# Kernel tuning notes

Measured on AMD Instinct MI355X. Metric: run time of the kernel, lower is better.

The kernel has to match this reference:

```python
import jax, jax.numpy as jnp
import numpy as np

B, C, H, W, HEADS, S = 8, 512, 32, 32, 8, 77
CH = C // HEADS  # per-head channels = 64
GROUPS = 32      # GroupNorm32


def setup_inputs() -> dict:
    key = jax.random.key(0)
    ks = jax.random.split(key, 6)
    s = 0.02
    return {
        "x": jax.random.normal(ks[0], (B, C, H, W), jnp.float32),
        "encoder_out": jax.random.normal(ks[1], (B, C, S), jnp.float32),
        "capt_attn_mask": jax.random.bernoulli(ks[2], 0.9, (B, S)),
        "norm_scale": jnp.ones((C,), jnp.float32),
        "norm_bias": jnp.zeros((C,), jnp.float32),
        "qkv_w": jax.random.normal(ks[3], (3 * C, C), jnp.float32) * s,
        "qkv_b": jnp.zeros((3 * C,), jnp.float32),
        "ekv_w": jax.random.normal(ks[4], (2 * C, C), jnp.float32) * s,
        "ekv_b": jnp.zeros((2 * C,), jnp.float32),
        "proj_w": jax.random.normal(ks[5], (C, C), jnp.float32) * s,
        "proj_b": jnp.zeros((C,), jnp.float32),
    }


def reference(x, encoder_out, capt_attn_mask, norm_scale, norm_bias,
              qkv_w, qkv_b, ekv_w, ekv_b, proj_w, proj_b):
    b, c, h, w = x.shape
    T = h * w
    xf = x.reshape(b, c, T)

    # GroupNorm(32) in fp32 (GroupNorm32), affine
    xg = xf.reshape(b, GROUPS, c // GROUPS, T).astype(jnp.float32)
    mu = xg.mean(axis=(2, 3), keepdims=True)
    var = xg.var(axis=(2, 3), keepdims=True)
    nrm = ((xg - mu) * jax.lax.rsqrt(var + 1e-5)).reshape(b, c, T)
    nrm = nrm * norm_scale[None, :, None] + norm_bias[None, :, None]

    # 1x1 conv1d qkv projection: [b, 3c, T]
    qkv = jnp.einsum('oc,bct->bot', qkv_w, nrm) + qkv_b[None, :, None]
    qkv = qkv.reshape(b * HEADS, 3 * CH, T)
    q, k, v = jnp.split(qkv, 3, axis=1)  # each [b*heads, CH, T]

    # encoder kv: [b, 2c, S] -> [b*heads, 2*CH, S]
    ekv = jnp.einsum('oc,bcs->bos', ekv_w, encoder_out) + ekv_b[None, :, None]
    ekv = ekv.reshape(b * HEADS, 2 * CH, S)
    ek, ev = jnp.split(ekv, 2, axis=1)
    k = jnp.concatenate([ek, k], axis=-1)  # [b*heads, CH, S+T]
    v = jnp.concatenate([ev, v], axis=-1)

    scale = 1.0 / np.sqrt(np.sqrt(CH))
    wgt = jnp.einsum('bct,bcs->bts', q * scale, k * scale).astype(jnp.float32)

    # additive mask; torch.tile over dim0 is head-major (row i -> batch i % b),
    # faithfully reproduced; self-attn part (last T cols) is all-visible.
    addm_capt = jnp.where(jnp.tile(capt_attn_mask, (HEADS, 1)), 0.0, -10000.0)
    addm = jnp.concatenate(
        [addm_capt, jnp.zeros((b * HEADS, T), jnp.float32)], axis=1)[:, None, :]
    wgt = jax.nn.softmax(wgt + addm, axis=-1).astype(v.dtype)

    out = jnp.einsum('bts,bcs->bct', wgt, v)  # [b*heads, CH, T]
    out = out.reshape(b, c, T)
    out = jnp.einsum('oc,bct->bot', proj_w, out) + proj_b[None, :, None]
    return (xf + out).reshape(b, c, h, w)
```

## Files before the change

kernel.cpp:

```cpp
#include <hip/hip_runtime.h>
#include <math.h>

#define BB 8
#define TT 1024
#define SS 77

typedef short v8s __attribute__((ext_vector_type(8)));
typedef float v4f __attribute__((ext_vector_type(4)));
typedef unsigned short u16x4 __attribute__((ext_vector_type(4)));
typedef unsigned short u16x8 __attribute__((ext_vector_type(8)));
typedef unsigned short u16;

#define SCALEF 0.424660891f
#define MASKNEG (-14426.95f)

__device__ __forceinline__ u16 f2bf(float f) {
  unsigned u = __float_as_uint(f);
  u = (u + 0x7fffu + ((u >> 16) & 1u)) >> 16;
  return (u16)u;
}
__device__ __forceinline__ u16 hi16(float f) {
  return (u16)(__float_as_uint(f) >> 16);
}
__device__ __forceinline__ float bf2f(u16 u) {
  return __uint_as_float(((unsigned)u) << 16);
}
__device__ __forceinline__ void gl_lds16(const void* g, void* l) {
  __builtin_amdgcn_global_load_lds(
      (const __attribute__((address_space(1))) void*)g,
      (__attribute__((address_space(3))) void*)l, 16, 0, 0);
}

__global__ __launch_bounds__(256) void prep_gn_kernel(
    const float* __restrict__ x, const float* __restrict__ scale,
    const float* __restrict__ bias, u16* __restrict__ nrmT,
    const float* __restrict__ qkv_w, const float* __restrict__ ekv_w,
    const float* __restrict__ proj_w, const float* __restrict__ enc,
    const float* __restrict__ qkv_b, const float* __restrict__ ekv_b,
    u16* __restrict__ wQK, u16* __restrict__ wV, u16* __restrict__ wEK,
    u16* __restrict__ wEV, u16* __restrict__ projwb, u16* __restrict__ encT,
    float* __restrict__ bQK, float* __restrict__ bV,
    float* __restrict__ bEK, float* __restrict__ bEV) {
  __shared__ u16 Xs[16 * 1024];
  __shared__ float red[8];
  int blk = blockIdx.x, tid = threadIdx.x;

  if (blk < 256) {
    int bg = blk;
    int b = bg >> 5, g = bg & 31;
    const float4* x4 = (const float4*)(x + (size_t)bg * 16384);
    float s = 0.f, sq = 0.f;
#pragma unroll
    for (int i = 0; i < 16; ++i) {
      int idx = tid + 256 * i;
      float4 v = x4[idx];
      s += v.x + v.y + v.z + v.w;
      sq += v.x * v.x + v.y * v.y + v.z * v.z + v.w * v.w;
      int c = idx >> 8, t4 = (idx & 255) * 4;
      u16x4 o; o.x = f2bf(v.x); o.y = f2bf(v.y); o.z = f2bf(v.z); o.w = f2bf(v.w);
      *(u16x4*)(Xs + c * 1024 + t4) = o;
    }
#pragma unroll
    for (int off = 32; off > 0; off >>= 1) {
      s += __shfl_down(s, off, 64);
      sq += __shfl_down(sq, off, 64);
    }
    int wave = tid >> 6;
    if ((tid & 63) == 0) { red[wave] = s; red[wave + 4] = sq; }
    __syncthreads();
    float ts = red[0] + red[1] + red[2] + red[3];
    float tq = red[4] + red[5] + red[6] + red[7];
    float mu = ts * (1.0f / 16384.0f);
    float var = tq * (1.0f / 16384.0f) - mu * mu;
    float rs = rsqrtf(var + 1e-5f);
    float scv[16], biv[16];
#pragma unroll
    for (int c = 0; c < 16; ++c) {
      float ss = scale[g * 16 + c] * rs;
      scv[c] = ss;
      biv[c] = bias[g * 16 + c] - mu * ss;
    }
#pragma unroll
    for (int j = 0; j < 4; ++j) {
      int t = tid + 256 * j;
      u16x8 o0, o1;
#pragma unroll
      for (int c = 0; c < 8; ++c)  o0[c] = f2bf(bf2f(Xs[c * 1024 + t]) * scv[c] + biv[c]);
#pragma unroll
      for (int c = 8; c < 16; ++c) o1[c - 8] = f2bf(bf2f(Xs[c * 1024 + t]) * scv[c] + biv[c]);
      u16* dst = nrmT + ((size_t)b * 1024 + t) * 512 + g * 16;
      *(u16x8*)dst = o0;
      *(u16x8*)(dst + 8) = o1;
    }
    return;
  }

  int p = blk - 256;
  if (p < 512) {
    int idx = p * 256 + tid;
    int n = idx >> 7, c4 = (idx & 127) * 4;
    int which = n >> 9, h = (n >> 6) & 7, ch = n & 63;
    int src = h * 192 + which * 64 + ch;
    float4 v = *(const float4*)(qkv_w + (size_t)src * 512 + c4);
    u16x4 o; o.x = f2bf(v.x * SCALEF); o.y = f2bf(v.y * SCALEF);
    o.z = f2bf(v.z * SCALEF); o.w = f2bf(v.w * SCALEF);
    *(u16x4*)(wQK + (size_t)n * 512 + c4) = o;
  } else if (p < 768) {
    int idx = (p - 512) * 256 + tid;
    int n = idx >> 7, c4 = (idx & 127) * 4;
    int h = n >> 6, ch = n & 63;
    int src = h * 192 + 128 + ch;
    float4 v = *(const float4*)(qkv_w + (size_t)src * 512 + c4);
    u16x4 o; o.x = f2bf(v.x); o.y = f2bf(v.y); o.z = f2bf(v.z); o.w = f2bf(v.w);
    *(u16x4*)(wV + (size_t)n * 512 + c4) = o;
  } else if (p < 1024) {
    int idx = (p - 768) * 256 + tid;
    int n = idx >> 7, c4 = (idx & 127) * 4;
    int h = n >> 6, ch = n & 63;
    int src = h * 128 + ch;
    float4 v = *(const float4*)(ekv_w + (size_t)src * 512 + c4);
    u16x4 o; o.x = f2bf(v.x * SCALEF); o.y = f2bf(v.y * SCALEF);
    o.z = f2bf(v.z * SCALEF); o.w = f2bf(v.w * SCALEF);
    *(u16x4*)(wEK + (size_t)n * 512 + c4) = o;
  } else if (p < 1280) {
    int idx = (p - 1024) * 256 + tid;
    int n = idx >> 7, c4 = (idx & 127) * 4;
    int h = n >> 6, ch = n & 63;
    int src = h * 128 + 64 + ch;
    float4 v = *(const float4*)(ekv_w + (size_t)src * 512 + c4);
    u16x4 o; o.x = f2bf(v.x); o.y = f2bf(v.y); o.z = f2bf(v.z); o.w = f2bf(v.w);
    *(u16x4*)(wEV + (size_t)n * 512 + c4) = o;
  } else if (p < 1536) {
    int idx = (p - 1280) * 256 + tid;
    float4 v = ((const float4*)proj_w)[idx];
    u16x4 o; o.x = f2bf(v.x); o.y = f2bf(v.y); o.z = f2bf(v.z); o.w = f2bf(v.w);
    *(u16x4*)(projwb + (size_t)idx * 4) = o;
  } else if (p < 2048) {
    int idx = (p - 1536) * 256 + tid;
    int b = idx >> 14, rem = idx & 16383;
    int s = rem >> 7, c = (rem & 127) * 4;
    u16x4 o; o.x = 0; o.y = 0; o.z = 0; o.w = 0;
    if (s < SS) {
      const float* pp = enc + ((size_t)b * 512 + c) * SS + s;
      o.x = f2bf(pp[0]); o.y = f2bf(pp[SS]); o.z = f2bf(pp[2 * SS]); o.w = f2bf(pp[3 * SS]);
    }
    *(u16x4*)(encT + ((size_t)b * 128 + s) * 512 + c) = o;
  } else {
    for (int i = tid; i < 2560; i += 256) {
      if (i < 1024) {
        int which = i >> 9, h = (i >> 6) & 7, ch = i & 63;
        bQK[i] = qkv_b[h * 192 + which * 64 + ch] * SCALEF;
      } else if (i < 1536) {
        int j = i - 1024; int h = j >> 6, ch = j & 63;
        bV[j] = qkv_b[h * 192 + 128 + ch];
      } else if (i < 2048) {
        int j = i - 1536; int h = j >> 6, ch = j & 63;
        bEK[j] = ekv_b[h * 128 + ch] * SCALEF;
      } else {
        int j = i - 2048; int h = j >> 6, ch = j & 63;
        bEV[j] = ekv_b[h * 128 + 64 + ch];
      }
    }
  }
}

__global__ __launch_bounds__(256) void proj_all(
    const u16* __restrict__ nrmT, const u16* __restrict__ encT,
    const u16* __restrict__ wQK, const u16* __restrict__ wEK,
    const u16* __restrict__ wV, const u16* __restrict__ wEV,
    const float* __restrict__ bQK, const float* __restrict__ bEK,
    const float* __restrict__ bV, const float* __restrict__ bEV,
    u16* __restrict__ Qh, u16* __restrict__ Kfull, u16* __restrict__ Vfull) {
  __shared__ __align__(16) u16 SH[16384];
  u16* As = SH;
  u16* Bs = SH + 8192;

  int job = blockIdx.x, bz = blockIdx.y;
  int tid = threadIdx.x;
  int lane = tid & 63, w = tid >> 6;
  int lan15 = lane & 15, quad = lane >> 4;
  int wm = w >> 1, wn = w & 1;

  int mode, m0, n0;
  const u16 *Ap, *Bp;
  const float* bias;
  u16 *dA = nullptr, *dB = nullptr;
  int TrA = 0, offA = 0, TrB = 0, offB = 0;
  int coff = 0;

  if (job < 64) {
    mode = 3; m0 = (job >> 3) * 128; n0 = (job & 7) * 128;
    Ap = nrmT + (size_t)bz * 1024 * 512; Bp = wQK; bias = bQK;
    dA = Qh; TrA = 1024; offA = 0; dB = Kfull; TrB = 1152; offB = 128;
  } else if (job < 68) {
    mode = 3; m0 = 0; n0 = (job - 64) * 128;
    Ap = encT + (size_t)bz * 128 * 512; Bp = wEK; bias = bEK;
    dA = Kfull; TrA = 1152; offA = 0; dB = Kfull; TrB = 1152; offB = 0;
  } else if (job < 100) {
    int jj = job - 68; mode = 0; m0 = (jj >> 3) * 128; n0 = (jj & 7) * 128;
    Ap = wV; Bp = nrmT + (size_t)bz * 1024 * 512; bias = bV;
    coff = 128;
  } else {
    int jj = job - 100; mode = 0; m0 = jj * 128; n0 = 0;
    Ap = wEV; Bp = encT + (size_t)bz * 128 * 512; bias = bEV;
    coff = 0;
  }

  int srow = lane >> 3;
  int schunk = (lane & 7) ^ srow;
  const char* Ag = (const char*)(Ap + (size_t)(m0 + w * 32 + srow) * 512) + schunk * 16;
  const char* Bg = (const char*)(Bp + (size_t)(n0 + w * 32 + srow) * 512) + schunk * 16;
  char* Al = (char*)As + w * 4096;
  char* Bl = (char*)Bs + w * 4096;

  v4f acc[4][4] = {};

  for (int step = 0; step < 8; ++step) {
    __syncthreads();
    int kb = step * 128;
#pragma unroll
    for (int i = 0; i < 4; ++i) gl_lds16(Ag + kb + i * 8192, Al + i * 1024);
#pragma unroll
    for (int i = 0; i < 4; ++i) gl_lds16(Bg + kb + i * 8192, Bl + i * 1024);
    __syncthreads();

#pragma unroll
    for (int ksub = 0; ksub < 2; ++ksub) {
      int ch = ((ksub * 4 + quad) ^ (lan15 & 7)) * 16;
      v8s a[4], bf[4];
#pragma unroll
      for (int i = 0; i < 4; ++i)
        a[i] = *(const v8s*)((const char*)As + (wm * 64 + i * 16 + lan15) * 128 + ch);
#pragma unroll
      for (int j = 0; j < 4; ++j)
        bf[j] = *(const v8s*)((const char*)Bs + (wn * 64 + j * 16 + lan15) * 128 + ch);
#pragma unroll
      for (int i = 0; i < 4; ++i)
#pragma unroll
        for (int j = 0; j < 4; ++j)
          acc[i][j] = __builtin_amdgcn_mfma_f32_16x16x32_bf16(a[i], bf[j], acc[i][j], 0, 0, 0);
    }
  }

  if (mode == 3) {
    u16* Tr = SH;
    for (int ph = 0; ph < 2; ++ph) {
      __syncthreads();
      if (wn == ph) {
#pragma unroll
        for (int j = 0; j < 4; ++j) {
          int n = n0 + wn * 64 + j * 16 + lan15;
          float bv_ = bias[n];
#pragma unroll
          for (int i = 0; i < 4; ++i)
#pragma unroll
            for (int r = 0; r < 4; ++r)
              Tr[(wm * 64 + i * 16 + quad * 4 + r) * 72 + j * 16 + lan15] =
                  f2bf(acc[i][j][r] + bv_);
        }
      }
      __syncthreads();
      int nb = n0 + ph * 64;
      u16* dst = (nb < 512) ? dA : dB;
      int Trows = (nb < 512) ? TrA : TrB;
      int roff  = (nb < 512) ? offA : offB;
      int hh = (nb & 511) >> 6;
      int row = tid >> 1, seg = (tid & 1) * 32;
      u16* dp = dst + ((size_t)(bz * 8 + hh) * Trows + roff + m0 + row) * 64 + seg;
#pragma unroll
      for (int g = 0; g < 4; ++g)
        *(u16x8*)(dp + g * 8) = *(const u16x8*)(Tr + row * 72 + seg + g * 8);
    }
  } else {
    u16* Tr = SH;
    u16* Cb = Vfull + (size_t)bz * 512 * 1152;
    for (int ph = 0; ph < 2; ++ph) {
      __syncthreads();
      if (wn == ph) {
#pragma unroll
        for (int i = 0; i < 4; ++i) {
          int ob = wm * 64 + i * 16 + quad * 4;
#pragma unroll
          for (int r = 0; r < 4; ++r) {
            float bi = bias[m0 + ob + r];
#pragma unroll
            for (int j = 0; j < 4; ++j)
              Tr[(ob + r) * 72 + j * 16 + lan15] = f2bf(acc[i][j][r] + bi);
          }
        }
      }
      __syncthreads();
      int row = tid >> 1, seg = (tid & 1) * 32;
      u16* dp = Cb + (size_t)(m0 + row) * 1152 + coff + n0 + ph * 64 + seg;
#pragma unroll
      for (int g = 0; g < 4; ++g)
        *(u16x8*)(dp + g * 8) = *(const u16x8*)(Tr + row * 72 + seg + g * 8);
    }
  }
}

__global__ __launch_bounds__(256) void proj_out(
    const u16* __restrict__ A, const u16* __restrict__ B,
    const float* __restrict__ bias, const float* __restrict__ res,
    float* __restrict__ Cf) {
  __shared__ __align__(16) u16 SH[16384];
  u16* As = SH;
  u16* Bs = SH + 8192;

  int tid = threadIdx.x;
  int lane = tid & 63, w = tid >> 6;
  int lan15 = lane & 15, quad = lane >> 4;
  int wm = w >> 1, wn = w & 1;
  int m0 = blockIdx.y * 128, n0 = blockIdx.x * 128;
  int bz = blockIdx.z;
  const u16* Bb = B + (size_t)bz * 1024 * 512;

  int srow = lane >> 3;
  int schunk = (lane & 7) ^ srow;
  const char* Ag = (const char*)(A + (size_t)(m0 + w * 32 + srow) * 512) + schunk * 16;
  const char* Bg = (const char*)(Bb + (size_t)(n0 + w * 32 + srow) * 512) + schunk * 16;
  char* Al = (char*)As + w * 4096;
  char* Bl = (char*)Bs + w * 4096;

  v4f acc[4][4] = {};

  for (int step = 0; step < 8; ++step) {
    __syncthreads();
    int kb = step * 128;
#pragma unroll
    for (int i = 0; i < 4; ++i) gl_lds16(Ag + kb + i * 8192, Al + i * 1024);
#pragma unroll
    for (int i = 0; i < 4; ++i) gl_lds16(Bg + kb + i * 8192, Bl + i * 1024);
    __syncthreads();

#pragma unroll
    for (int ksub = 0; ksub < 2; ++ksub) {
      int ch = ((ksub * 4 + quad) ^ (lan15 & 7)) * 16;
      v8s a[4], bf[4];
#pragma unroll
      for (int i = 0; i < 4; ++i)
        a[i] = *(const v8s*)((const char*)As + (wm * 64 + i * 16 + lan15) * 128 + ch);
#pragma unroll
      for (int j = 0; j < 4; ++j)
        bf[j] = *(const v8s*)((const char*)Bs + (wn * 64 + j * 16 + lan15) * 128 + ch);
#pragma unroll
      for (int i = 0; i < 4; ++i)
#pragma unroll
        for (int j = 0; j < 4; ++j)
          acc[i][j] = __builtin_amdgcn_mfma_f32_16x16x32_bf16(a[i], bf[j], acc[i][j], 0, 0, 0);
    }
  }

  const float* rb = res + (size_t)bz * 512 * 1024;
  float* Cb = Cf + (size_t)bz * 512 * 1024;
#pragma unroll
  for (int i = 0; i < 4; ++i) {
    int ob = m0 + wm * 64 + i * 16 + quad * 4;
#pragma unroll
    for (int r = 0; r < 4; ++r) {
      int o = ob + r;
      float bi = bias[o];
#pragma unroll
      for (int j = 0; j < 4; ++j) {
        int n = n0 + wn * 64 + j * 16 + lan15;
        Cb[(size_t)o * 1024 + n] = acc[i][j][r] + bi + rb[(size_t)o * 1024 + n];
      }
    }
  }
}

#define AOFF_K 0
#define AOFF_V 24576
#define AOFF_P 49152
#define AOFF_AM 67584
#define ASMEM  68096

__global__ __launch_bounds__(256) void attn_kernel(
    const u16* __restrict__ Qh, const u16* __restrict__ Kf,
    const u16* __restrict__ Vf, const int* __restrict__ mask,
    u16* __restrict__ attnT) {
  __shared__ __align__(16) unsigned char smem[ASMEM];
  float* AM = (float*)(smem + AOFF_AM);

  int bh = blockIdx.x, b = bh >> 3, h = bh & 7;
  int t0 = blockIdx.y * 128;
  int tid = threadIdx.x;
  int lane = tid & 63, w = tid >> 6;
  int lan15 = lane & 15, quad = lane >> 4;
  int r8 = lane >> 3, c8 = lane & 7;
  int swE = (c8 ^ r8) * 8;

  const u16* Qb = Qh + (size_t)bh * 1024 * 64;
  const u16* Kb = Kf + (size_t)bh * 1152 * 64;
  const u16* Vb = Vf + (size_t)bh * 64 * 1152;
  char* Pw = (char*)smem + AOFF_P + w * 4608;
  u16* Pu = (u16*)Pw;

  if (tid < 128)
    AM[tid] = (tid < SS) ? ((mask[h * SS + tid] != 0) ? 0.f : MASKNEG) : -1e30f;

#pragma unroll
  for (int i = 0; i < 4; ++i)
    gl_lds16(Qb + (size_t)(t0 + w * 32 + i * 8 + r8) * 64 + swE, Pw + i * 1024);
#pragma unroll
  for (int cc = 0; cc < 2; ++cc) {
#pragma unroll
    for (int i = 0; i < 2; ++i) {
      int row = w * 16 + i * 8;
      gl_lds16(Kb + (size_t)(cc * 64 + row + r8) * 64 + swE,
               (char*)smem + AOFF_K + cc * 8192 + row * 128);
      gl_lds16(Vb + (size_t)(row + r8) * 1152 + cc * 64 + swE,
               (char*)smem + AOFF_V + cc * 8192 + row * 128);
    }
  }

  asm volatile("s_waitcnt vmcnt(8)" ::: "memory");
  __builtin_amdgcn_sched_barrier(0);

  v8s aq[2][2];
#pragma unroll
  for (int mt = 0; mt < 2; ++mt)
#pragma unroll
    for (int ks = 0; ks < 2; ++ks)
      aq[mt][ks] = *(const v8s*)(Pw + (mt * 16 + lan15) * 128 +
                                 (((ks * 4 + quad) ^ (lan15 & 7)) * 16));

  asm volatile("s_waitcnt vmcnt(4) lgkmcnt(0)" ::: "memory");
  __builtin_amdgcn_sched_barrier(0);
  __builtin_amdgcn_s_barrier();
  __builtin_amdgcn_sched_barrier(0);

  v4f O[2][4] = {};
  float lsum[2] = {0.f, 0.f};
  int cur = 0;

  for (int c = 0; c < 18; ++c) {
    if (c < 16) {
      int nb = cur + 2; if (nb >= 3) nb -= 3;
#pragma unroll
      for (int i = 0; i < 2; ++i) {
        int row = w * 16 + i * 8;
        gl_lds16(Kb + (size_t)((c + 2) * 64 + row + r8) * 64 + swE,
                 (char*)smem + AOFF_K + nb * 8192 + row * 128);
        gl_lds16(Vb + (size_t)(row + r8) * 1152 + (c + 2) * 64 + swE,
                 (char*)smem + AOFF_V + nb * 8192 + row * 128);
      }
    }
    const char* Kc = (const char*)smem + AOFF_K + cur * 8192;
    const char* Vc = (const char*)smem + AOFF_V + cur * 8192;

    v4f ST[4][2] = {};
#pragma unroll
    for (int ks = 0; ks < 2; ++ks) {
      int cofs = ((ks * 4 + quad) ^ (lan15 & 7)) * 16;
      v8s bk[4];
#pragma unroll
      for (int nt = 0; nt < 4; ++nt)
        bk[nt] = *(const v8s*)(Kc + (nt * 16 + lan15) * 128 + cofs);
      __builtin_amdgcn_s_setprio(1);
#pragma unroll
      for (int nt = 0; nt < 4; ++nt)
#pragma unroll
        for (int mt = 0; mt < 2; ++mt)
          ST[nt][mt] = __builtin_amdgcn_mfma_f32_16x16x32_bf16(bk[nt], aq[mt][ks], ST[nt][mt], 0, 0, 0);
      __builtin_amdgcn_s_setprio(0);
    }

    if (c < 2) {
#pragma unroll
      for (int nt = 0; nt < 4; ++nt)
#pragma unroll
        for (int r = 0; r < 4; ++r) {
          float a_ = AM[c * 64 + nt * 16 + quad * 4 + r];
#pragma unroll
          for (int mt = 0; mt < 2; ++mt) ST[nt][mt][r] += a_;
        }
    }

#pragma unroll
    for (int mt = 0; mt < 2; ++mt) {
#pragma unroll
      for (int nt = 0; nt < 4; ++nt) {
        float e0 = __builtin_amdgcn_exp2f(ST[nt][mt][0]);
        float e1 = __builtin_amdgcn_exp2f(ST[nt][mt][1]);
        float e2 = __builtin_amdgcn_exp2f(ST[nt][mt][2]);
        float e3 = __builtin_amdgcn_exp2f(ST[nt][mt][3]);
        u16x4 pk; pk.x = hi16(e0); pk.y = hi16(e1); pk.z = hi16(e2); pk.w = hi16(e3);
        *(u16x4*)&Pu[(mt * 16 + lan15) * 72 + nt * 16 + quad * 4] = pk;
        lsum[mt] += (e0 + e1) + (e2 + e3);
      }
    }

#pragma unroll
    for (int ks = 0; ks < 2; ++ks) {
      int cofs = ((ks * 4 + quad) ^ (lan15 & 7)) * 16;
      v8s ap[2], bv[4];
#pragma unroll
      for (int mt = 0; mt < 2; ++mt)
        ap[mt] = *(const v8s*)(Pw + (mt * 16 + lan15) * 144 + ks * 64 + quad * 16);
#pragma unroll
      for (int nc = 0; nc < 4; ++nc)
        bv[nc] = *(const v8s*)(Vc + (nc * 16 + lan15) * 128 + cofs);
      __builtin_amdgcn_s_setprio(1);
#pragma unroll
      for (int mt = 0; mt < 2; ++mt)
#pragma unroll
        for (int nc = 0; nc < 4; ++nc)
          O[mt][nc] = __builtin_amdgcn_mfma_f32_16x16x32_bf16(ap[mt], bv[nc], O[mt][nc], 0, 0, 0);
      __builtin_amdgcn_s_setprio(0);
    }

    if (c < 17) {
      if (c < 16) asm volatile("s_waitcnt vmcnt(4)" ::: "memory");
      else        asm volatile("s_waitcnt vmcnt(0)" ::: "memory");
      __builtin_amdgcn_sched_barrier(0);
      __builtin_amdgcn_s_barrier();
      __builtin_amdgcn_sched_barrier(0);
    }
    cur = cur + 1; if (cur == 3) cur = 0;
  }

#pragma unroll
  for (int mt = 0; mt < 2; ++mt) {
    float v = lsum[mt];
    v += __shfl_xor(v, 16, 64);
    v += __shfl_xor(v, 32, 64);
    AM[w * 32 + mt * 16 + lan15] = v;
  }
  __syncthreads();
  float inv[2][4];
#pragma unroll
  for (int mt = 0; mt < 2; ++mt)
#pragma unroll
    for (int r = 0; r < 4; ++r)
      inv[mt][r] = 1.0f / AM[w * 32 + mt * 16 + quad * 4 + r];

  float* Ot = (float*)smem;
#pragma unroll
  for (int mt = 0; mt < 2; ++mt)
#pragma unroll
    for (int nc = 0; nc < 4; ++nc)
#pragma unroll
      for (int r = 0; r < 4; ++r)
        Ot[(w * 32 + mt * 16 + quad * 4 + r) * 68 + nc * 16 + lan15] =
            O[mt][nc][r] * inv[mt][r];
  __syncthreads();
  {
    int row = tid >> 1, seg = (tid & 1) * 32;
    const float* src = Ot + row * 68 + seg;
    u16* dp = attnT + ((size_t)b * 1024 + t0 + row) * 512 + h * 64 + seg;
#pragma unroll
    for (int g = 0; g < 4; ++g) {
      u16x8 o;
#pragma unroll
      for (int k = 0; k < 8; ++k) o[k] = f2bf(src[g * 8 + k]);
      *(u16x8*)(dp + g * 8) = o;
    }
  }
}

extern "C" void kernel_launch(void* const* d_in, const int* in_sizes, int n_in,
                              void* d_out, int out_size, void* d_ws, size_t ws_size,
                              hipStream_t stream) {
  const float* x       = (const float*)d_in[0];
  const float* enc     = (const float*)d_in[1];
  const int*   mask    = (const int*)d_in[2];
  const float* nscale  = (const float*)d_in[3];
  const float* nbias   = (const float*)d_in[4];
  const float* qkv_w   = (const float*)d_in[5];
  const float* qkv_b   = (const float*)d_in[6];
  const float* ekv_w   = (const float*)d_in[7];
  const float* ekv_b   = (const float*)d_in[8];
  const float* proj_w  = (const float*)d_in[9];
  const float* proj_b  = (const float*)d_in[10];
  float* out = (float*)d_out;

  char* ws = (char*)d_ws;
  const size_t MiB = 1048576;
  u16* nrmT   = (u16*)(ws);
  u16* Qh     = (u16*)(ws + 8 * MiB);
  u16* Kfull  = (u16*)(ws + 16 * MiB);
  u16* Vfull  = (u16*)(ws + 26 * MiB);
  u16* attnT  = (u16*)(ws + 36 * MiB);
  u16* encT   = (u16*)(ws + 44 * MiB);
  u16* wQK    = (u16*)(ws + 45 * MiB);
  u16* wV     = (u16*)(ws + 46 * MiB);
  u16* wEK    = (u16*)(ws + 46 * MiB + 524288);
  u16* wEV    = (u16*)(ws + 47 * MiB);
  u16* projwb = (u16*)(ws + 47 * MiB + 524288);
  float* bQK  = (float*)(ws + 48 * MiB);
  float* bV   = (float*)(ws + 48 * MiB + 4096);
  float* bEK  = (float*)(ws + 48 * MiB + 6144);
  float* bEV  = (float*)(ws + 48 * MiB + 8192);

  prep_gn_kernel<<<dim3(2305), dim3(256), 0, stream>>>(
      x, nscale, nbias, nrmT, qkv_w, ekv_w, proj_w, enc, qkv_b, ekv_b,
      wQK, wV, wEK, wEV, projwb, encT, bQK, bV, bEK, bEV);

  proj_all<<<dim3(104, BB), dim3(256), 0, stream>>>(
      nrmT, encT, wQK, wEK, wV, wEV, bQK, bEK, bV, bEV, Qh, Kfull, Vfull);

  attn_kernel<<<dim3(64, 8), dim3(256), 0, stream>>>(
      Qh, Kfull, Vfull, mask, attnT);

  proj_out<<<dim3(8, 4, BB), dim3(256), 0, stream>>>(
      projwb, attnT, proj_b, x, out);
}
```

Before: 173.8 us.

## Split attention block across eight waves with sixteen query rows each

The attention kernel now launches 512 threads per block, with each of eight wavefronts handling 16 query rows instead of 32. K/V tile loads are spread across the eight waves, and the per-wave P scratch shrinks to match. The goal is more waves per CU to hide latency and less register pressure per wave. The cost is less K/V fragment reuse per wave: each K/V LDS read now feeds half as many MFMAs, so LDS traffic per FLOP goes up.

```diff
diff --git a/kernel.cpp b/kernel.cpp
--- a/kernel.cpp
+++ b/kernel.cpp
@@ -375,7 +375,7 @@
 #define AOFF_AM 67584
 #define ASMEM  68096
 
-__global__ __launch_bounds__(256) void attn_kernel(
+__global__ __launch_bounds__(512, 4) void attn_kernel(
     const u16* __restrict__ Qh, const u16* __restrict__ Kf,
     const u16* __restrict__ Vf, const int* __restrict__ mask,
     u16* __restrict__ attnT) {
@@ -393,63 +393,55 @@
   const u16* Qb = Qh + (size_t)bh * 1024 * 64;
   const u16* Kb = Kf + (size_t)bh * 1152 * 64;
   const u16* Vb = Vf + (size_t)bh * 64 * 1152;
-  char* Pw = (char*)smem + AOFF_P + w * 4608;
+  char* Pw = (char*)smem + AOFF_P + w * 2304;
   u16* Pu = (u16*)Pw;
 
   if (tid < 128)
     AM[tid] = (tid < SS) ? ((mask[h * SS + tid] != 0) ? 0.f : MASKNEG) : -1e30f;
 
 #pragma unroll
-  for (int i = 0; i < 4; ++i)
-    gl_lds16(Qb + (size_t)(t0 + w * 32 + i * 8 + r8) * 64 + swE, Pw + i * 1024);
+  for (int i = 0; i < 2; ++i)
+    gl_lds16(Qb + (size_t)(t0 + w * 16 + i * 8 + r8) * 64 + swE, Pw + i * 1024);
 #pragma unroll
   for (int cc = 0; cc < 2; ++cc) {
-#pragma unroll
-    for (int i = 0; i < 2; ++i) {
-      int row = w * 16 + i * 8;
-      gl_lds16(Kb + (size_t)(cc * 64 + row + r8) * 64 + swE,
-               (char*)smem + AOFF_K + cc * 8192 + row * 128);
-      gl_lds16(Vb + (size_t)(row + r8) * 1152 + cc * 64 + swE,
-               (char*)smem + AOFF_V + cc * 8192 + row * 128);
-    }
-  }
-
-  asm volatile("s_waitcnt vmcnt(8)" ::: "memory");
+    int row = w * 8;
+    gl_lds16(Kb + (size_t)(cc * 64 + row + r8) * 64 + swE,
+             (char*)smem + AOFF_K + cc * 8192 + row * 128);
+    gl_lds16(Vb + (size_t)(row + r8) * 1152 + cc * 64 + swE,
+             (char*)smem + AOFF_V + cc * 8192 + row * 128);
+  }
+
+  asm volatile("s_waitcnt vmcnt(4)" ::: "memory");
   __builtin_amdgcn_sched_barrier(0);
 
-  v8s aq[2][2];
-#pragma unroll
-  for (int mt = 0; mt < 2; ++mt)
-#pragma unroll
-    for (int ks = 0; ks < 2; ++ks)
-      aq[mt][ks] = *(const v8s*)(Pw + (mt * 16 + lan15) * 128 +
-                                 (((ks * 4 + quad) ^ (lan15 & 7)) * 16));
-
-  asm volatile("s_waitcnt vmcnt(4) lgkmcnt(0)" ::: "memory");
+  v8s aq[2];
+#pragma unroll
+  for (int ks = 0; ks < 2; ++ks)
+    aq[ks] = *(const v8s*)(Pw + lan15 * 128 +
+                           (((ks * 4 + quad) ^ (lan15 & 7)) * 16));
+
+  asm volatile("s_waitcnt vmcnt(2) lgkmcnt(0)" ::: "memory");
   __builtin_amdgcn_sched_barrier(0);
   __builtin_amdgcn_s_barrier();
   __builtin_amdgcn_sched_barrier(0);
 
-  v4f O[2][4] = {};
-  float lsum[2] = {0.f, 0.f};
+  v4f O[4] = {};
+  float lsum = 0.f;
   int cur = 0;
 
   for (int c = 0; c < 18; ++c) {
     if (c < 16) {
       int nb = cur + 2; if (nb >= 3) nb -= 3;
-#pragma unroll
-      for (int i = 0; i < 2; ++i) {
-        int row = w * 16 + i * 8;
-        gl_lds16(Kb + (size_t)((c + 2) * 64 + row + r8) * 64 + swE,
-                 (char*)smem + AOFF_K + nb * 8192 + row * 128);
-        gl_lds16(Vb + (size_t)(row + r8) * 1152 + (c + 2) * 64 + swE,
-                 (char*)smem + AOFF_V + nb * 8192 + row * 128);
-      }
+      int row = w * 8;
+      gl_lds16(Kb + (size_t)((c + 2) * 64 + row + r8) * 64 + swE,
+               (char*)smem + AOFF_K + nb * 8192 + row * 128);
+      gl_lds16(Vb + (size_t)(row + r8) * 1152 + (c + 2) * 64 + swE,
+               (char*)smem + AOFF_V + nb * 8192 + row * 128);
     }
     const char* Kc = (const char*)smem + AOFF_K + cur * 8192;
     const char* Vc = (const char*)smem + AOFF_V + cur * 8192;
 
-    v4f ST[4][2] = {};
+    v4f ST[4] = {};
 #pragma unroll
     for (int ks = 0; ks < 2; ++ks) {
       int cofs = ((ks * 4 + quad) ^ (lan15 & 7)) * 16;
@@ -460,9 +452,7 @@
       __builtin_amdgcn_s_setprio(1);
 #pragma unroll
       for (int nt = 0; nt < 4; ++nt)
-#pragma unroll
-        for (int mt = 0; mt < 2; ++mt)
-          ST[nt][mt] = __builtin_amdgcn_mfma_f32_16x16x32_bf16(bk[nt], aq[mt][ks], ST[nt][mt], 0, 0, 0);
+        ST[nt] = __builtin_amdgcn_mfma_f32_16x16x32_bf16(bk[nt], aq[ks], ST[nt], 0, 0, 0);
       __builtin_amdgcn_s_setprio(0);
     }
 
@@ -470,48 +460,38 @@
 #pragma unroll
       for (int nt = 0; nt < 4; ++nt)
 #pragma unroll
-        for (int r = 0; r < 4; ++r) {
-          float a_ = AM[c * 64 + nt * 16 + quad * 4 + r];
-#pragma unroll
-          for (int mt = 0; mt < 2; ++mt) ST[nt][mt][r] += a_;
-        }
-    }
-
-#pragma unroll
-    for (int mt = 0; mt < 2; ++mt) {
-#pragma unroll
-      for (int nt = 0; nt < 4; ++nt) {
-        float e0 = __builtin_amdgcn_exp2f(ST[nt][mt][0]);
-        float e1 = __builtin_amdgcn_exp2f(ST[nt][mt][1]);
-        float e2 = __builtin_amdgcn_exp2f(ST[nt][mt][2]);
-        float e3 = __builtin_amdgcn_exp2f(ST[nt][mt][3]);
-        u16x4 pk; pk.x = hi16(e0); pk.y = hi16(e1); pk.z = hi16(e2); pk.w = hi16(e3);
-        *(u16x4*)&Pu[(mt * 16 + lan15) * 72 + nt * 16 + quad * 4] = pk;
-        lsum[mt] += (e0 + e1) + (e2 + e3);
-      }
+        for (int r = 0; r < 4; ++r)
+          ST[nt][r] += AM[c * 64 + nt * 16 + quad * 4 + r];
+    }
+
+#pragma unroll
+    for (int nt = 0; nt < 4; ++nt) {
+      float e0 = __builtin_amdgcn_exp2f(ST[nt][0]);
+      float e1 = __builtin_amdgcn_exp2f(ST[nt][1]);
+      float e2 = __builtin_amdgcn_exp2f(ST[nt][2]);
+      float e3 = __builtin_amdgcn_exp2f(ST[nt][3]);
+      u16x4 pk; pk.x = hi16(e0); pk.y = hi16(e1); pk.z = hi16(e2); pk.w = hi16(e3);
+      *(u16x4*)&Pu[lan15 * 72 + nt * 16 + quad * 4] = pk;
+      lsum += (e0 + e1) + (e2 + e3);
     }
 
 #pragma unroll
     for (int ks = 0; ks < 2; ++ks) {
       int cofs = ((ks * 4 + quad) ^ (lan15 & 7)) * 16;
-      v8s ap[2], bv[4];
-#pragma unroll
-      for (int mt = 0; mt < 2; ++mt)
-        ap[mt] = *(const v8s*)(Pw + (mt * 16 + lan15) * 144 + ks * 64 + quad * 16);
+      v8s ap, bv[4];
+      ap = *(const v8s*)(Pw + lan15 * 144 + ks * 64 + quad * 16);
 #pragma unroll
       for (int nc = 0; nc < 4; ++nc)
         bv[nc] = *(const v8s*)(Vc + (nc * 16 + lan15) * 128 + cofs);
       __builtin_amdgcn_s_setprio(1);
 #pragma unroll
-      for (int mt = 0; mt < 2; ++mt)
-#pragma unroll
-        for (int nc = 0; nc < 4; ++nc)
-          O[mt][nc] = __builtin_amdgcn_mfma_f32_16x16x32_bf16(ap[mt], bv[nc], O[mt][nc], 0, 0, 0);
+      for (int nc = 0; nc < 4; ++nc)
+        O[nc] = __builtin_amdgcn_mfma_f32_16x16x32_bf16(ap, bv[nc], O[nc], 0, 0, 0);
       __builtin_amdgcn_s_setprio(0);
     }
 
     if (c < 17) {
-      if (c < 16) asm volatile("s_waitcnt vmcnt(4)" ::: "memory");
+      if (c < 16) asm volatile("s_waitcnt vmcnt(2)" ::: "memory");
       else        asm volatile("s_waitcnt vmcnt(0)" ::: "memory");
       __builtin_amdgcn_sched_barrier(0);
       __builtin_amdgcn_s_barrier();
@@ -520,37 +500,31 @@
     cur = cur + 1; if (cur == 3) cur = 0;
   }
 
-#pragma unroll
-  for (int mt = 0; mt < 2; ++mt) {
-    float v = lsum[mt];
+  {
+    float v = lsum;
     v += __shfl_xor(v, 16, 64);
     v += __shfl_xor(v, 32, 64);
-    AM[w * 32 + mt * 16 + lan15] = v;
+    AM[w * 16 + lan15] = v;
   }
   __syncthreads();
-  float inv[2][4];
-#pragma unroll
-  for (int mt = 0; mt < 2; ++mt)
+  float inv[4];
+#pragma unroll
+  for (int r = 0; r < 4; ++r)
+    inv[r] = 1.0f / AM[w * 16 + quad * 4 + r];
+
+  float* Ot = (float*)smem;
+#pragma unroll
+  for (int nc = 0; nc < 4; ++nc)
 #pragma unroll
     for (int r = 0; r < 4; ++r)
-      inv[mt][r] = 1.0f / AM[w * 32 + mt * 16 + quad * 4 + r];
-
-  float* Ot = (float*)smem;
-#pragma unroll
-  for (int mt = 0; mt < 2; ++mt)
-#pragma unroll
-    for (int nc = 0; nc < 4; ++nc)
-#pragma unroll
-      for (int r = 0; r < 4; ++r)
-        Ot[(w * 32 + mt * 16 + quad * 4 + r) * 68 + nc * 16 + lan15] =
-            O[mt][nc][r] * inv[mt][r];
+      Ot[(w * 16 + quad * 4 + r) * 68 + nc * 16 + lan15] = O[nc][r] * inv[r];
   __syncthreads();
   {
-    int row = tid >> 1, seg = (tid & 1) * 32;
+    int row = tid >> 2, seg = (tid & 3) * 16;
     const float* src = Ot + row * 68 + seg;
     u16* dp = attnT + ((size_t)b * 1024 + t0 + row) * 512 + h * 64 + seg;
 #pragma unroll
-    for (int g = 0; g < 4; ++g) {
+    for (int g = 0; g < 2; ++g) {
       u16x8 o;
 #pragma unroll
       for (int k = 0; k < 8; ++k) o[k] = f2bf(src[g * 8 + k]);
@@ -600,7 +574,7 @@
   proj_all<<<dim3(104, BB), dim3(256), 0, stream>>>(
       nrmT, encT, wQK, wEK, wV, wEV, bQK, bEK, bV, bEV, Qh, Kfull, Vfull);
 
-  attn_kernel<<<dim3(64, 8), dim3(256), 0, stream>>>(
+  attn_kernel<<<dim3(64, 8), dim3(512), 0, stream>>>(
       Qh, Kfull, Vfull, mask, attnT);
 
   proj_out<<<dim3(8, 4, BB), dim3(256), 0, stream>>>(
```

Result: no change. 172.5 us (-0.7%).
